# Kernel tuning notes

Hardware: AMD Instinct MI355X
Metric: run time of the kernel (lower is better)

Reference implementation:

```python
import jax, jax.numpy as jnp
import numpy as np

N_USER = 100000
N_RECIPE = 50000
E = 1000000
H = 128


def setup_inputs() -> dict:
    key = jax.random.key(0)
    ks = jax.random.split(key, 5)
    z_user = jax.random.normal(ks[0], (N_USER, H), dtype=jnp.float32)
    z_recipe = jax.random.normal(ks[1], (N_RECIPE, H), dtype=jnp.float32)
    edge_label_index = jax.random.randint(ks[2], (2, E), 0, N_RECIPE, dtype=jnp.int64)
    W1 = jax.random.normal(ks[3], (2 * H, H), dtype=jnp.float32) * (1.0 / np.sqrt(2 * H))
    b1 = jnp.zeros((H,), dtype=jnp.float32)
    W2 = jax.random.normal(ks[4], (H, 1), dtype=jnp.float32) * (1.0 / np.sqrt(H))
    b2 = jnp.zeros((1,), dtype=jnp.float32)
    return {"z_user": z_user, "z_recipe": z_recipe,
            "edge_label_index": edge_label_index,
            "W1": W1, "b1": b1, "W2": W2, "b2": b2}


def reference(z_user, z_recipe, edge_label_index, W1, b1, W2, b2):
    row, col = edge_label_index[0], edge_label_index[1]
    # gather + concat: [E, 2H]
    z = jnp.concatenate([z_user[row], z_recipe[col]], axis=-1)
    h = jax.nn.relu(z @ W1 + b1)        # [E, H]
    out = h @ W2 + b2                    # [E, 1]
    return out.reshape(-1)
```

## Files before the change

### kernel.cpp

```cpp
#include <hip/hip_runtime.h>
#include <hip/hip_bf16.h>


#define HDIM 128

typedef __attribute__((ext_vector_type(8))) __bf16 bf16x8;
typedef __attribute__((ext_vector_type(16))) float f32x16;

static __device__ __forceinline__ unsigned short bf16_bits(float x) {
  return __builtin_bit_cast(unsigned short, static_cast<__bf16>(x));
}

static __device__ __forceinline__ float bf2f(unsigned short u) {
  return __builtin_bit_cast(float, ((unsigned int)u) << 16);
}

static __device__ __forceinline__ bf16x8 cvt8(float4 a, float4 b) {
  bf16x8 r;
  r[0] = static_cast<__bf16>(a.x);
  r[1] = static_cast<__bf16>(a.y);
  r[2] = static_cast<__bf16>(a.z);
  r[3] = static_cast<__bf16>(a.w);
  r[4] = static_cast<__bf16>(b.x);
  r[5] = static_cast<__bf16>(b.y);
  r[6] = static_cast<__bf16>(b.z);
  r[7] = static_cast<__bf16>(b.w);
  return r;
}

__global__ __launch_bounds__(256, 2) void proj_nodes(
    const float* __restrict__ zu, int NU, const float* __restrict__ zr, int NR,
    const float* __restrict__ W1, unsigned short* __restrict__ Hu,
    unsigned short* __restrict__ Hr) {
  __shared__ unsigned short Bsw[32768];
  const int tid = threadIdx.x;
  {
    const int n = tid & 127;
    const int kh = tid >> 7;
    const int nt = n >> 5;
    const int nl = n & 31;
#pragma unroll 8
    for (int it = 0; it < 128; ++it) {
      const int k = 2 * it + kh;
      const float w = W1[k * HDIM + n];
      const int kc = k >> 4;
      const int q = (k >> 3) & 1;
      const int j = k & 7;
      const int ln = (q << 5) | nl;
      Bsw[((((kc << 2) + nt) << 6) | ln) * 8 + j] = bf16_bits(w);
    }
  }
  __syncthreads();

  const int lane = tid & 63;
  const int wid = tid >> 6;
  const int m = lane & 31;
  const int half = lane >> 5;
  const int koff = half * 8;
  const int utiles = NU >> 5;
  const int rtiles = (NR + 31) >> 5;
  const int ntiles = utiles + rtiles;
  const int wstride = gridDim.x * 4;

  for (int t = blockIdx.x * 4 + wid; t < ntiles; t += wstride) {
    const bool isU = t < utiles;
    const int base = isU ? (t << 5) : ((t - utiles) << 5);
    const int nmax = isU ? NU : NR;
    int node = base + m;
    if (node >= nmax) node = nmax - 1;
    const float* src = (isU ? zu : zr) + (size_t)node * HDIM + koff;
    const int kc0 = isU ? 0 : 8;

    f32x16 acc[4];
#pragma unroll
    for (int nt = 0; nt < 4; ++nt) acc[nt] = (f32x16)0.0f;

#pragma unroll
    for (int kcl = 0; kcl < 8; ++kcl) {
      const float4* sa = (const float4*)(src + kcl * 16);
      const bf16x8 a = cvt8(sa[0], sa[1]);
#pragma unroll
      for (int nt = 0; nt < 4; ++nt) {
        const uint4* bp =
            (const uint4*)(Bsw + (((((kc0 + kcl) << 2) + nt) << 6) | lane) * 8);
        const bf16x8 bfr = __builtin_bit_cast(bf16x8, *bp);
        acc[nt] = __builtin_amdgcn_mfma_f32_32x32x16_bf16(a, bfr, acc[nt], 0, 0, 0);
      }
    }

    unsigned short* H = isU ? Hu : Hr;
#pragma unroll
    for (int nt = 0; nt < 4; ++nt) {
#pragma unroll
      for (int r = 0; r < 16; ++r) {
        const int row = (r & 3) + ((r >> 2) << 3) + (half << 2);
        const int nrow = base + row;
        if (nrow < nmax)
          H[(size_t)nrow * HDIM + (nt << 5) + m] = bf16_bits(acc[nt][r]);
      }
    }
  }
}

static __device__ __forceinline__ float dot8(uint4 a, uint4 b,
                                             const float* b1c,
                                             const float* w2c) {
  const unsigned short* pa = (const unsigned short*)&a;
  const unsigned short* pb = (const unsigned short*)&b;
  float s = 0.f;
#pragma unroll
  for (int j = 0; j < 8; ++j) {
    const float h = bf2f(pa[j]) + bf2f(pb[j]) + b1c[j];
    s = fmaf(fmaxf(h, 0.f), w2c[j], s);
  }
  return s;
}

__global__ __launch_bounds__(256, 4) void edge_pass(
    const unsigned short* __restrict__ Hu, const unsigned short* __restrict__ Hr,
    const int* __restrict__ eidx, const float* __restrict__ b1,
    const float* __restrict__ W2, const float* __restrict__ b2,
    float* __restrict__ out, int E) {
  const int tid = threadIdx.x;
  const int lane = tid & 63;
  const int c = lane & 15;
  const int g = lane >> 4;
  const int wid = blockIdx.x * 4 + (tid >> 6);
  const int stride = gridDim.x * 4 * 8;

  float b1c[8], w2c[8];
#pragma unroll
  for (int j = 0; j < 8; ++j) {
    b1c[j] = b1[c * 8 + j];
    w2c[j] = W2[c * 8 + j];
  }
  const float b2v = b2[0];

  int e = wid * 8 + g * 2;
  if (e >= E) return;
  int iu0 = eidx[e], ir0 = eidx[E + e];
  int iu1 = eidx[e + 1], ir1 = eidx[E + e + 1];

  while (true) {
    const int en = e + stride;
    const bool more = en < E;
    const int ep = more ? en : e;

    const uint4 au0 = *(const uint4*)(Hu + (size_t)iu0 * HDIM + c * 8);
    const uint4 ar0 = *(const uint4*)(Hr + (size_t)ir0 * HDIM + c * 8);
    const uint4 au1 = *(const uint4*)(Hu + (size_t)iu1 * HDIM + c * 8);
    const uint4 ar1 = *(const uint4*)(Hr + (size_t)ir1 * HDIM + c * 8);

    const int niu0 = eidx[ep], nir0 = eidx[E + ep];
    const int niu1 = eidx[ep + 1], nir1 = eidx[E + ep + 1];

    float s0 = dot8(au0, ar0, b1c, w2c);
    float s1 = dot8(au1, ar1, b1c, w2c);
#pragma unroll
    for (int st = 1; st <= 8; st <<= 1) {
      s0 += __shfl_xor(s0, st);
      s1 += __shfl_xor(s1, st);
    }
    if (c == 0) {
      out[e] = s0 + b2v;
      out[e + 1] = s1 + b2v;
    }
    if (!more) break;
    e = en;
    iu0 = niu0; ir0 = nir0; iu1 = niu1; ir1 = nir1;
  }
}

__global__ __launch_bounds__(256, 2) void edge_decoder_mfma(
    const float* __restrict__ zu, const float* __restrict__ zr,
    const int* __restrict__ eidx, const float* __restrict__ W1,
    const float* __restrict__ b1, const float* __restrict__ W2,
    const float* __restrict__ b2, float* __restrict__ out, int E) {
  __shared__ unsigned short Bsw[32768];
  const int tid = threadIdx.x;
  {
    const int n = tid & 127;
    const int kh = tid >> 7;
    const int nt = n >> 5;
    const int nl = n & 31;
#pragma unroll 8
    for (int it = 0; it < 128; ++it) {
      const int k = 2 * it + kh;
      const float w = W1[k * HDIM + n];
      const int kc = k >> 4;
      const int q = (k >> 3) & 1;
      const int j = k & 7;
      const int ln = (q << 5) | nl;
      Bsw[((((kc << 2) + nt) << 6) | ln) * 8 + j] = bf16_bits(w);
    }
  }
  __syncthreads();

  const int lane = tid & 63;
  const int wid = tid >> 6;
  const int m = lane & 31;
  const int half = lane >> 5;
  const int nsweep = E >> 6;
  const int wstride = gridDim.x * 4;

  float b1v[4], w2v[4];
#pragma unroll
  for (int nt = 0; nt < 4; ++nt) {
    b1v[nt] = b1[nt * 32 + m];
    w2v[nt] = W2[nt * 32 + m];
  }
  const float b2v = b2[0];
  const int koff = half * 8;

  for (int s = blockIdx.x * 4 + wid; s < nsweep; s += wstride) {
    const int e0 = s << 6;
    const int eA = e0 + m;
    const int eB = e0 + 32 + m;
    const float* puA = zu + (size_t)eidx[eA] * HDIM;
    const float* prA = zr + (size_t)eidx[E + eA] * HDIM;
    const float* puB = zu + (size_t)eidx[eB] * HDIM;
    const float* prB = zr + (size_t)eidx[E + eB] * HDIM;

    f32x16 acc[2][4];
#pragma unroll
    for (int mt = 0; mt < 2; ++mt)
#pragma unroll
      for (int nt = 0; nt < 4; ++nt) acc[mt][nt] = (f32x16)0.0f;

#pragma unroll
    for (int kc = 0; kc < 16; ++kc) {
      const float* srcA = (kc < 8) ? (puA + kc * 16 + koff) : (prA + (kc - 8) * 16 + koff);
      const float* srcB = (kc < 8) ? (puB + kc * 16 + koff) : (prB + (kc - 8) * 16 + koff);
      const float4* sa = (const float4*)srcA;
      const float4* sb = (const float4*)srcB;
      const bf16x8 a0 = cvt8(sa[0], sa[1]);
      const bf16x8 a1 = cvt8(sb[0], sb[1]);
#pragma unroll
      for (int nt = 0; nt < 4; ++nt) {
        const uint4* bp = (const uint4*)(Bsw + ((((kc << 2) + nt) << 6) | lane) * 8);
        const bf16x8 bfr = __builtin_bit_cast(bf16x8, *bp);
        acc[0][nt] = __builtin_amdgcn_mfma_f32_32x32x16_bf16(a0, bfr, acc[0][nt], 0, 0, 0);
        acc[1][nt] = __builtin_amdgcn_mfma_f32_32x32x16_bf16(a1, bfr, acc[1][nt], 0, 0, 0);
      }
    }

    float p0[16], p1[16];
#pragma unroll
    for (int r = 0; r < 16; ++r) { p0[r] = 0.f; p1[r] = 0.f; }
#pragma unroll
    for (int nt = 0; nt < 4; ++nt) {
#pragma unroll
      for (int r = 0; r < 16; ++r) {
        float h0 = fmaxf(acc[0][nt][r] + b1v[nt], 0.f);
        float h1 = fmaxf(acc[1][nt][r] + b1v[nt], 0.f);
        p0[r] = fmaf(h0, w2v[nt], p0[r]);
        p1[r] = fmaf(h1, w2v[nt], p1[r]);
      }
    }
#pragma unroll
    for (int st = 1; st <= 16; st <<= 1) {
#pragma unroll
      for (int r = 0; r < 16; ++r) {
        p0[r] += __shfl_xor(p0[r], st);
        p1[r] += __shfl_xor(p1[r], st);
      }
    }
    const int sel = lane & 15;
    const int mtw = (lane >> 4) & 1;
    float val = 0.f;
#pragma unroll
    for (int r = 0; r < 16; ++r) {
      const float cand = mtw ? p1[r] : p0[r];
      val = (sel == r) ? cand : val;
    }
    const int mrow = (sel & 3) + ((sel >> 2) << 3) + (half << 2);
    out[e0 + (mtw << 5) + mrow] = val + b2v;
  }
}

extern "C" void kernel_launch(void* const* d_in, const int* in_sizes, int n_in,
                              void* d_out, int out_size, void* d_ws,
                              size_t ws_size, hipStream_t stream) {
  const float* zu = (const float*)d_in[0];
  const float* zr = (const float*)d_in[1];
  const int* eidx = (const int*)d_in[2];
  const float* W1 = (const float*)d_in[3];
  const float* b1 = (const float*)d_in[4];
  const float* W2 = (const float*)d_in[5];
  const float* b2 = (const float*)d_in[6];
  float* out = (float*)d_out;
  const int nu = in_sizes[0];
  const int nr = in_sizes[1];
  const int E = in_sizes[2] / 2;
  const int NU = nu / HDIM, NR = nr / HDIM;

  const size_t need = (size_t)(nu + nr) * sizeof(unsigned short);
  if (ws_size >= need) {
    unsigned short* Hu = (unsigned short*)d_ws;
    unsigned short* Hr = Hu + (size_t)nu;
    hipLaunchKernelGGL(proj_nodes, dim3(512), dim3(256), 0, stream,
                       zu, NU, zr, NR, W1, Hu, Hr);
    hipLaunchKernelGGL(edge_pass, dim3(2048), dim3(256), 0, stream,
                       Hu, Hr, eidx, b1, W2, b2, out, E);
  } else {
    hipLaunchKernelGGL(edge_decoder_mfma, dim3(512), dim3(256), 0, stream,
                       zu, zr, eidx, W1, b1, W2, b2, out, E);
  }
}
```

Measured before the change: 196.5 us.

## Pre-swizzle W1 once, split projection by node type, widen edge unroll

Adds a small prep kernel that converts and swizzles W1 into bf16 once in workspace. proj_nodes now launches one block per four 32-node tiles, each block handling only user or recipe nodes, and copies only the half of W1 it needs into shared memory. This halves LDS use and allows more blocks per CU, at the cost of a larger grid and one extra kernel launch. The edge pass now processes four edges per 16-lane group instead of two, putting more gathers in flight per wave.

```diff
diff --git a/kernel.cpp b/kernel.cpp
--- a/kernel.cpp
+++ b/kernel.cpp
@@ -28,24 +28,50 @@
   return r;
 }
 
-__global__ __launch_bounds__(256, 2) void proj_nodes(
+__global__ void prep_w1(const float* __restrict__ W1,
+                        unsigned short* __restrict__ W1bf) {
+  const int tid = threadIdx.x;
+#pragma unroll
+  for (int it = 0; it < 8; ++it) {
+    const int idx = (blockIdx.x << 11) + (it << 8) + tid;
+    const int k = idx >> 7;
+    const int n = idx & 127;
+    const int kc = k >> 4;
+    const int q = (k >> 3) & 1;
+    const int j = k & 7;
+    const int nt = n >> 5;
+    const int ln = (q << 5) | (n & 31);
+    W1bf[((((kc << 2) + nt) << 6) | ln) * 8 + j] = bf16_bits(W1[idx]);
+  }
+}
+
+__global__ __launch_bounds__(256, 4) void proj_nodes(
     const float* __restrict__ zu, int NU, const float* __restrict__ zr, int NR,
-    const float* __restrict__ W1, unsigned short* __restrict__ Hu,
-    unsigned short* __restrict__ Hr) {
-  __shared__ unsigned short Bsw[32768];
+    const float* __restrict__ W1, const unsigned short* __restrict__ W1bf,
+    unsigned short* __restrict__ Hu, unsigned short* __restrict__ Hr,
+    int ublocks) {
+  __shared__ unsigned short Bsw[16384];
   const int tid = threadIdx.x;
-  {
+  const bool isU = (int)blockIdx.x < ublocks;
+  const int kc0 = isU ? 0 : 8;
+
+  if (W1bf) {
+    const uint4* s4 = (const uint4*)(W1bf + (kc0 << 11));
+    uint4* d4 = (uint4*)Bsw;
+#pragma unroll
+    for (int i = 0; i < 8; ++i) d4[(i << 8) + tid] = s4[(i << 8) + tid];
+  } else {
     const int n = tid & 127;
     const int kh = tid >> 7;
     const int nt = n >> 5;
     const int nl = n & 31;
 #pragma unroll 8
-    for (int it = 0; it < 128; ++it) {
-      const int k = 2 * it + kh;
-      const float w = W1[k * HDIM + n];
-      const int kc = k >> 4;
-      const int q = (k >> 3) & 1;
-      const int j = k & 7;
+    for (int it = 0; it < 64; ++it) {
+      const int kl = 2 * it + kh;
+      const float w = W1[(kc0 * 16 + kl) * HDIM + n];
+      const int kc = kl >> 4;
+      const int q = (kl >> 3) & 1;
+      const int j = kl & 7;
       const int ln = (q << 5) | nl;
       Bsw[((((kc << 2) + nt) << 6) | ln) * 8 + j] = bf16_bits(w);
     }
@@ -57,47 +83,43 @@
   const int m = lane & 31;
   const int half = lane >> 5;
   const int koff = half * 8;
-  const int utiles = NU >> 5;
-  const int rtiles = (NR + 31) >> 5;
-  const int ntiles = utiles + rtiles;
-  const int wstride = gridDim.x * 4;
-
-  for (int t = blockIdx.x * 4 + wid; t < ntiles; t += wstride) {
-    const bool isU = t < utiles;
-    const int base = isU ? (t << 5) : ((t - utiles) << 5);
-    const int nmax = isU ? NU : NR;
-    int node = base + m;
-    if (node >= nmax) node = nmax - 1;
-    const float* src = (isU ? zu : zr) + (size_t)node * HDIM + koff;
-    const int kc0 = isU ? 0 : 8;
-
-    f32x16 acc[4];
-#pragma unroll
-    for (int nt = 0; nt < 4; ++nt) acc[nt] = (f32x16)0.0f;
-
-#pragma unroll
-    for (int kcl = 0; kcl < 8; ++kcl) {
-      const float4* sa = (const float4*)(src + kcl * 16);
-      const bf16x8 a = cvt8(sa[0], sa[1]);
-#pragma unroll
-      for (int nt = 0; nt < 4; ++nt) {
-        const uint4* bp =
-            (const uint4*)(Bsw + (((((kc0 + kcl) << 2) + nt) << 6) | lane) * 8);
-        const bf16x8 bfr = __builtin_bit_cast(bf16x8, *bp);
-        acc[nt] = __builtin_amdgcn_mfma_f32_32x32x16_bf16(a, bfr, acc[nt], 0, 0, 0);
-      }
-    }
-
-    unsigned short* H = isU ? Hu : Hr;
+
+  const int tl = (isU ? (int)blockIdx.x : (int)blockIdx.x - ublocks) * 4 + wid;
+  const int ntype = isU ? ((NU + 31) >> 5) : ((NR + 31) >> 5);
+  if (tl >= ntype) return;
+
+  const int base = tl << 5;
+  const int nmax = isU ? NU : NR;
+  int node = base + m;
+  if (node >= nmax) node = nmax - 1;
+  const float* src = (isU ? zu : zr) + (size_t)node * HDIM + koff;
+
+  f32x16 acc[4];
+#pragma unroll
+  for (int nt = 0; nt < 4; ++nt) acc[nt] = (f32x16)0.0f;
+
+#pragma unroll
+  for (int kcl = 0; kcl < 8; ++kcl) {
+    const float4* sa = (const float4*)(src + kcl * 16);
+    const bf16x8 a = cvt8(sa[0], sa[1]);
 #pragma unroll
     for (int nt = 0; nt < 4; ++nt) {
-#pragma unroll
-      for (int r = 0; r < 16; ++r) {
-        const int row = (r & 3) + ((r >> 2) << 3) + (half << 2);
-        const int nrow = base + row;
-        if (nrow < nmax)
-          H[(size_t)nrow * HDIM + (nt << 5) + m] = bf16_bits(acc[nt][r]);
-      }
+      const uint4* bp =
+          (const uint4*)(Bsw + ((((kcl << 2) + nt) << 6) | lane) * 8);
+      const bf16x8 bfr = __builtin_bit_cast(bf16x8, *bp);
+      acc[nt] = __builtin_amdgcn_mfma_f32_32x32x16_bf16(a, bfr, acc[nt], 0, 0, 0);
+    }
+  }
+
+  unsigned short* H = isU ? Hu : Hr;
+#pragma unroll
+  for (int nt = 0; nt < 4; ++nt) {
+#pragma unroll
+    for (int r = 0; r < 16; ++r) {
+      const int row = (r & 3) + ((r >> 2) << 3) + (half << 2);
+      const int nrow = base + row;
+      if (nrow < nmax)
+        H[(size_t)nrow * HDIM + (nt << 5) + m] = bf16_bits(acc[nt][r]);
     }
   }
 }
@@ -126,7 +148,7 @@
   const int c = lane & 15;
   const int g = lane >> 4;
   const int wid = blockIdx.x * 4 + (tid >> 6);
-  const int stride = gridDim.x * 4 * 8;
+  const int stride = gridDim.x * 4 * 16;
 
   float b1c[8], w2c[8];
 #pragma unroll
@@ -135,39 +157,55 @@
     w2c[j] = W2[c * 8 + j];
   }
   const float b2v = b2[0];
-
-  int e = wid * 8 + g * 2;
+  const int co = c * 8;
+
+  int e = wid * 16 + g * 4;
   if (e >= E) return;
-  int iu0 = eidx[e], ir0 = eidx[E + e];
+  int iu0 = eidx[e],     ir0 = eidx[E + e];
   int iu1 = eidx[e + 1], ir1 = eidx[E + e + 1];
+  int iu2 = eidx[e + 2], ir2 = eidx[E + e + 2];
+  int iu3 = eidx[e + 3], ir3 = eidx[E + e + 3];
 
   while (true) {
     const int en = e + stride;
     const bool more = en < E;
     const int ep = more ? en : e;
 
-    const uint4 au0 = *(const uint4*)(Hu + (size_t)iu0 * HDIM + c * 8);
-    const uint4 ar0 = *(const uint4*)(Hr + (size_t)ir0 * HDIM + c * 8);
-    const uint4 au1 = *(const uint4*)(Hu + (size_t)iu1 * HDIM + c * 8);
-    const uint4 ar1 = *(const uint4*)(Hr + (size_t)ir1 * HDIM + c * 8);
-
-    const int niu0 = eidx[ep], nir0 = eidx[E + ep];
+    const uint4 au0 = *(const uint4*)(Hu + (size_t)iu0 * HDIM + co);
+    const uint4 ar0 = *(const uint4*)(Hr + (size_t)ir0 * HDIM + co);
+    const uint4 au1 = *(const uint4*)(Hu + (size_t)iu1 * HDIM + co);
+    const uint4 ar1 = *(const uint4*)(Hr + (size_t)ir1 * HDIM + co);
+    const uint4 au2 = *(const uint4*)(Hu + (size_t)iu2 * HDIM + co);
+    const uint4 ar2 = *(const uint4*)(Hr + (size_t)ir2 * HDIM + co);
+    const uint4 au3 = *(const uint4*)(Hu + (size_t)iu3 * HDIM + co);
+    const uint4 ar3 = *(const uint4*)(Hr + (size_t)ir3 * HDIM + co);
+
+    const int niu0 = eidx[ep],     nir0 = eidx[E + ep];
     const int niu1 = eidx[ep + 1], nir1 = eidx[E + ep + 1];
+    const int niu2 = eidx[ep + 2], nir2 = eidx[E + ep + 2];
+    const int niu3 = eidx[ep + 3], nir3 = eidx[E + ep + 3];
 
     float s0 = dot8(au0, ar0, b1c, w2c);
     float s1 = dot8(au1, ar1, b1c, w2c);
+    float s2 = dot8(au2, ar2, b1c, w2c);
+    float s3 = dot8(au3, ar3, b1c, w2c);
 #pragma unroll
     for (int st = 1; st <= 8; st <<= 1) {
       s0 += __shfl_xor(s0, st);
       s1 += __shfl_xor(s1, st);
+      s2 += __shfl_xor(s2, st);
+      s3 += __shfl_xor(s3, st);
     }
     if (c == 0) {
-      out[e] = s0 + b2v;
+      out[e]     = s0 + b2v;
       out[e + 1] = s1 + b2v;
+      out[e + 2] = s2 + b2v;
+      out[e + 3] = s3 + b2v;
     }
     if (!more) break;
     e = en;
     iu0 = niu0; ir0 = nir0; iu1 = niu1; ir1 = nir1;
+    iu2 = niu2; ir2 = nir2; iu3 = niu3; ir3 = nir3;
   }
 }
 
@@ -294,12 +332,23 @@
   const int E = in_sizes[2] / 2;
   const int NU = nu / HDIM, NR = nr / HDIM;
 
-  const size_t need = (size_t)(nu + nr) * sizeof(unsigned short);
-  if (ws_size >= need) {
+  const size_t needH = (size_t)(nu + nr) * sizeof(unsigned short);
+  const size_t needW = 32768 * sizeof(unsigned short);
+
+  if (ws_size >= needH) {
     unsigned short* Hu = (unsigned short*)d_ws;
     unsigned short* Hr = Hu + (size_t)nu;
-    hipLaunchKernelGGL(proj_nodes, dim3(512), dim3(256), 0, stream,
-                       zu, NU, zr, NR, W1, Hu, Hr);
+    unsigned short* W1bf = nullptr;
+    if (ws_size >= needH + needW) {
+      W1bf = Hr + (size_t)nr;
+      hipLaunchKernelGGL(prep_w1, dim3(16), dim3(256), 0, stream, W1, W1bf);
+    }
+    const int utiles = (NU + 31) >> 5;
+    const int rtiles = (NR + 31) >> 5;
+    const int ub = (utiles + 3) >> 2;
+    const int rb = (rtiles + 3) >> 2;
+    hipLaunchKernelGGL(proj_nodes, dim3(ub + rb), dim3(256), 0, stream,
+                       zu, NU, zr, NR, W1, W1bf, Hu, Hr, ub);
     hipLaunchKernelGGL(edge_pass, dim3(2048), dim3(256), 0, stream,
                        Hu, Hr, eidx, b1, W2, b2, out, E);
   } else {
```

Measured after the change: 196.5 us. About the same (-0.0%).
